# Kernel tuning notes

Measured on AMD Instinct MI355X. Metric: run time of the kernel, lower is better.

## Reference

```python
import jax, jax.numpy as jnp
import numpy as np

B, C, N, K, L = 4, 256, 8192, 4, 3


def _mlp2(h, W1, b1, W2, b2):
    return jax.nn.relu(h @ W1 + b1) @ W2 + b2


def setup_inputs() -> dict:
    key = jax.random.key(0)
    ks = jax.random.split(key, 12)
    s = lambda fan_in: 1.0 / np.sqrt(fan_in)
    inp = {
        "x": jax.random.normal(ks[0], (B, C, N), jnp.float32),
        "points": jax.random.normal(ks[1], (N, 3), jnp.float32),
        "neighbors": jax.random.randint(ks[2], (N, K), 0, N, jnp.int32),
        "edge_W1": jax.random.normal(ks[3], (3, C // 4), jnp.float32) * s(3),
        "edge_b1": jnp.zeros((C // 4,), jnp.float32),
        "edge_W2": jax.random.normal(ks[4], (C // 4, C // 2), jnp.float32) * s(C // 4),
        "edge_b2": jnp.zeros((C // 2,), jnp.float32),
        "msg_W1": jax.random.normal(ks[5], (L, 2 * C + C // 2, 2 * C), jnp.float32) * s(2 * C + C // 2),
        "msg_b1": jnp.zeros((L, 2 * C), jnp.float32),
        "msg_W2": jax.random.normal(ks[6], (L, 2 * C, C), jnp.float32) * s(2 * C),
        "msg_b2": jnp.zeros((L, C), jnp.float32),
        "upd_W1": jax.random.normal(ks[7], (L, 2 * C, 2 * C), jnp.float32) * s(2 * C),
        "upd_b1": jnp.zeros((L, 2 * C), jnp.float32),
        "upd_W2": jax.random.normal(ks[8], (L, 2 * C, C), jnp.float32) * s(2 * C),
        "upd_b2": jnp.zeros((L, C), jnp.float32),
    }
    return inp


def reference(x, points, neighbors, edge_W1, edge_b1, edge_W2, edge_b2,
              msg_W1, msg_b1, msg_W2, msg_b2, upd_W1, upd_b1, upd_W2, upd_b2):
    # x: [B, C, N] -> features [B, N, C]
    feats = jnp.transpose(x, (0, 2, 1))
    # edge features shared across layers: [N, K, C//2]
    edge_vec = points[neighbors] - points[:, None, :]          # [N, K, 3]
    edge_feat = _mlp2(edge_vec, edge_W1, edge_b1, edge_W2, edge_b2)
    for l in range(L):
        sender = feats[:, neighbors, :]                         # [B, N, K, C]
        receiver = jnp.broadcast_to(feats[:, :, None, :], sender.shape)
        ef = jnp.broadcast_to(edge_feat[None], (feats.shape[0],) + edge_feat.shape)
        msg_in = jnp.concatenate([sender, receiver, ef], axis=-1)  # [B,N,K,2.5C]
        msg = _mlp2(msg_in, msg_W1[l], msg_b1[l], msg_W2[l], msg_b2[l])
        agg = jnp.mean(msg, axis=2)                             # [B, N, C]
        upd_in = jnp.concatenate([feats, agg], axis=-1)         # [B, N, 2C]
        feats = _mlp2(upd_in, upd_W1[l], upd_b1[l], upd_W2[l], upd_b2[l])
    return jnp.transpose(feats, (0, 2, 1))
```

## Files before the change

### kernel.cpp

```cpp
#include <hip/hip_runtime.h>

#define DEVI __device__ __forceinline__

typedef unsigned short u16;
typedef unsigned int   u32;
typedef __attribute__((ext_vector_type(8))) short short8;
typedef __attribute__((ext_vector_type(4))) short short4b;
typedef __attribute__((ext_vector_type(4))) float f32x4;

DEVI float bf2f(u16 u) {
    union { u32 i; float f; } x; x.i = ((u32)u) << 16; return x.f;
}
DEVI u16 f2bf(float f) {
    u32 u = __float_as_uint(f);
    u32 r = (u + 0x7FFFu + ((u >> 16) & 1u)) >> 16;
    return (u16)r;
}

DEVI void gload_lds16(const void* g, void* l) {
    __builtin_amdgcn_global_load_lds((const __attribute__((address_space(1))) void*)g,
                                     (__attribute__((address_space(3))) void*)l, 16, 0, 0);
}

struct PJob { u32 dst, soff, tbase, ld, Kd, src; };
__device__ const PJob g_jobs[19] = {
    {0,        0,      0,    128, 64,  4},
    {8192,     0,      8,    512, 256, 0},
    {139264,   131072, 136,  512, 256, 0},
    {270336,   262144, 264,  512, 128, 0},
    {335872,   0,      328,  256, 512, 1},
    {466944,   0,      456,  512, 512, 2},
    {729088,   0,      712,  256, 512, 3},
    {860160,   327680, 840,  512, 256, 0},
    {991232,   458752, 968,  512, 256, 0},
    {1122304,  589824, 1096, 512, 128, 0},
    {1187840,  131072, 1160, 256, 512, 1},
    {1318912,  262144, 1288, 512, 512, 2},
    {1581056,  131072, 1544, 256, 512, 3},
    {1712128,  655360, 1672, 512, 256, 0},
    {1843200,  786432, 1800, 512, 256, 0},
    {1974272,  917504, 1928, 512, 128, 0},
    {2039808,  262144, 1992, 256, 512, 1},
    {2170880,  524288, 2120, 512, 512, 2},
    {2433024,  262144, 2376, 256, 512, 3},
};

__global__ void prep_weights(const float* __restrict__ mW1, const float* __restrict__ mW2,
                             const float* __restrict__ uW1, const float* __restrict__ uW2,
                             const float* __restrict__ eW2, u16* __restrict__ wreg)
{
    int bid = blockIdx.x;
    int ji = 0;
    #pragma unroll
    for (int i = 1; i < 19; ++i) if (bid >= (int)g_jobs[i].tbase) ji = i;
    PJob jb = g_jobs[ji];
    const float* src = (jb.src == 0) ? mW1 : (jb.src == 1) ? mW2 : (jb.src == 2) ? uW1
                     : (jb.src == 3) ? uW2 : eW2;
    src += jb.soff;
    int t  = bid - (int)jb.tbase;
    int nk = (int)jb.Kd >> 5;
    int tk = t % nk, tj = t / nk;
    int k0 = tk * 32, j0 = tj * 32;
    __shared__ float tile[32][33];
    int tx = threadIdx.x, ty = threadIdx.y;
    #pragma unroll
    for (int yy = 0; yy < 4; ++yy) {
        int k = k0 + ty + yy * 8;
        tile[ty + yy * 8][tx] = src[(size_t)k * jb.ld + j0 + tx];
    }
    __syncthreads();
    u16* dst = wreg + jb.dst;
    #pragma unroll
    for (int yy = 0; yy < 4; ++yy) {
        int j = j0 + ty + yy * 8;
        dst[(size_t)j * jb.Kd + k0 + tx] = f2bf(tile[tx][ty + yy * 8]);
    }
}

__global__ __launch_bounds__(256) void conv_w2(const float* __restrict__ mW2,
                                               u16* __restrict__ mW2bf)
{
    int i = blockIdx.x * 256 + threadIdx.x;
    float4 v = *(const float4*)&mW2[(size_t)i * 4];
    short4b o;
    o[0] = (short)f2bf(v.x); o[1] = (short)f2bf(v.y);
    o[2] = (short)f2bf(v.z); o[3] = (short)f2bf(v.w);
    *(short4b*)&mW2bf[(size_t)i * 4] = o;
}

__global__ __launch_bounds__(256) void biasfix(const u16* __restrict__ wreg,
    const float* __restrict__ mb2, const float* __restrict__ ub1,
    float* __restrict__ ub1c)
{
    int idx = blockIdx.x * 256 + threadIdx.x;
    int l = idx >> 9, n = idx & 511;
    const u16* U1T = wreg + 8192 + l * 851968 + 458752;
    const float* b2 = mb2 + l * 256;
    float s = ub1[l * 512 + n];
    for (int j0 = 0; j0 < 256; j0 += 8) {
        short8 wv = *(const short8*)&U1T[(size_t)n * 512 + 256 + j0];
        #pragma unroll
        for (int jj = 0; jj < 8; ++jj) s += bf2f((u16)wv[jj]) * b2[j0 + jj];
    }
    ub1c[idx] = s;
}

__global__ void transpose_in(const float* __restrict__ x, u16* __restrict__ feats)
{
    __shared__ float tile[32][33];
    int n0 = blockIdx.x * 32, c0 = blockIdx.y * 32, b = blockIdx.z;
    int tx = threadIdx.x, ty = threadIdx.y;
    #pragma unroll
    for (int yy = 0; yy < 4; ++yy) {
        int c = c0 + ty + yy * 8;
        tile[ty + yy * 8][tx] = x[((size_t)b * 256 + c) * 8192 + n0 + tx];
    }
    __syncthreads();
    #pragma unroll
    for (int yy = 0; yy < 4; ++yy) {
        int n = n0 + ty + yy * 8;
        feats[((size_t)b * 8192 + n) * 256 + c0 + tx] = f2bf(tile[tx][ty + yy * 8]);
    }
}

__global__ void transpose_out(const u16* __restrict__ feats, float* __restrict__ out)
{
    __shared__ float tile[32][33];
    int n0 = blockIdx.x * 32, c0 = blockIdx.y * 32, b = blockIdx.z;
    int tx = threadIdx.x, ty = threadIdx.y;
    #pragma unroll
    for (int yy = 0; yy < 4; ++yy) {
        int n = n0 + ty + yy * 8;
        tile[ty + yy * 8][tx] = bf2f(feats[((size_t)b * 8192 + n) * 256 + c0 + tx]);
    }
    __syncthreads();
    #pragma unroll
    for (int yy = 0; yy < 4; ++yy) {
        int c = c0 + ty + yy * 8;
        out[((size_t)b * 256 + c) * 8192 + n0 + tx] = tile[tx][ty + yy * 8];
    }
}

__global__ __launch_bounds__(256) void edge_h(
    const float* __restrict__ points, const int* __restrict__ nb,
    const float* __restrict__ W1, const float* __restrict__ b1,
    u16* __restrict__ h)
{
    int e = blockIdx.x * 256 + threadIdx.x;
    int n = e >> 2;
    int j2 = nb[e];
    float p0x = points[n * 3], p0y = points[n * 3 + 1], p0z = points[n * 3 + 2];
    float v0 = points[j2 * 3]     - p0x;
    float v1 = points[j2 * 3 + 1] - p0y;
    float v2 = points[j2 * 3 + 2] - p0z;
    #pragma unroll
    for (int jb = 0; jb < 8; ++jb) {
        short8 o;
        #pragma unroll
        for (int jj = 0; jj < 8; ++jj) {
            int j = jb * 8 + jj;
            float hv = v0 * W1[j] + v1 * W1[64 + j] + v2 * W1[128 + j] + b1[j];
            o[jj] = (short)f2bf(fmaxf(hv, 0.0f));
        }
        *(short8*)&h[(size_t)e * 64 + jb * 8] = o;
    }
}

__global__ __launch_bounds__(256) void gemm_bt(
    const u16* __restrict__ A1, int lda1, int K1,
    const u16* __restrict__ A2, int lda2,
    const u16* __restrict__ B1, int ldb1,
    const u16* __restrict__ B2, int ldb2,
    const float* __restrict__ bias,
    u16* __restrict__ Cp, int ldc,
    int nbn, int Ktot, int relu)
{
    __shared__ u16 lds[128 * 136];
    u16* At = lds;
    u16* Bt = lds + 8192;
    int nwg = (int)gridDim.x;
    int bx0 = (int)blockIdx.x;
    int bx = (bx0 & 7) * (nwg >> 3) + (bx0 >> 3);
    int tn = bx % nbn, tm = bx / nbn;
    int t = threadIdx.x;
    int l = t & 63, w = t >> 6;
    int wrow = (w >> 1) * 64, wcol = (w & 1) * 64;
    int lm = l & 15, lk = l >> 4;
    int swz = lm & 7;

    f32x4 acc[4][4];
    #pragma unroll
    for (int mi = 0; mi < 4; ++mi)
        #pragma unroll
        for (int ni = 0; ni < 4; ++ni)
            acc[mi][ni] = (f32x4){0.f, 0.f, 0.f, 0.f};

    int rowA = tm * 128;
    int rowB = tn * 128;
    int nks = Ktot >> 6;
    for (int ks = 0; ks < nks; ++ks) {
        int kg0 = ks << 6;
        bool useA1 = kg0 < K1;
        const u16* Ab = useA1 ? A1 : A2;
        const u16* Bb = useA1 ? B1 : B2;
        int lda = useA1 ? lda1 : lda2;
        int ldb = useA1 ? ldb1 : ldb2;
        int kg  = useA1 ? kg0 : kg0 - K1;
        #pragma unroll
        for (int i = 0; i < 4; ++i) {
            int chunk = i * 256 + t;
            int r = chunk >> 3, s = chunk & 7;
            int c = s ^ (r & 7);
            gload_lds16(Ab + (size_t)(rowA + r) * lda + kg + c * 8, &At[chunk * 8]);
        }
        #pragma unroll
        for (int i = 0; i < 4; ++i) {
            int chunk = i * 256 + t;
            int r = chunk >> 3, s = chunk & 7;
            int c = s ^ (r & 7);
            gload_lds16(Bb + (size_t)(rowB + r) * ldb + kg + c * 8, &Bt[chunk * 8]);
        }
        __syncthreads();
        #pragma unroll
        for (int ksub = 0; ksub < 2; ++ksub) {
            int sOff = (((ksub << 2) | lk) ^ swz) << 3;
            short8 af[4], bv[4];
            #pragma unroll
            for (int mi = 0; mi < 4; ++mi)
                af[mi] = *(const short8*)&At[(wrow + mi * 16 + lm) * 64 + sOff];
            #pragma unroll
            for (int ni = 0; ni < 4; ++ni)
                bv[ni] = *(const short8*)&Bt[(wcol + ni * 16 + lm) * 64 + sOff];
            #pragma unroll
            for (int mi = 0; mi < 4; ++mi)
                #pragma unroll
                for (int ni = 0; ni < 4; ++ni)
                    acc[mi][ni] = __builtin_amdgcn_mfma_f32_16x16x32_bf16(af[mi], bv[ni], acc[mi][ni], 0, 0, 0);
        }
        __syncthreads();
    }

    #pragma unroll
    for (int ni = 0; ni < 4; ++ni) {
        int col = wcol + ni * 16 + lm;
        float bvl = bias ? bias[tn * 128 + col] : 0.0f;
        #pragma unroll
        for (int mi = 0; mi < 4; ++mi) {
            int row0 = wrow + mi * 16 + lk * 4;
            f32x4 v = acc[mi][ni];
            #pragma unroll
            for (int r = 0; r < 4; ++r) {
                float f = v[r] + bvl;
                if (relu) f = fmaxf(f, 0.0f);
                lds[(row0 + r) * 136 + col] = f2bf(f);
            }
        }
    }
    __syncthreads();
    #pragma unroll
    for (int p = 0; p < 8; ++p) {
        int chunk = p * 256 + t;
        int row = chunk >> 4, sl = chunk & 15;
        short8 v = *(const short8*)&lds[row * 136 + sl * 8];
        *(short8*)&Cp[(size_t)(tm * 128 + row) * ldc + tn * 128 + sl * 8] = v;
    }
}

__global__ __launch_bounds__(256) void gather_relu_mean(
    const u16* __restrict__ PR, const u16* __restrict__ E,
    const int* __restrict__ nb, const float* __restrict__ b1,
    u16* __restrict__ hbar)
{
    int b = threadIdx.x >> 6, l = threadIdx.x & 63;
    int c0 = l * 8;
    int n0 = blockIdx.x * 4;

    float4 b1a = *(const float4*)&b1[c0];
    float4 b1b = *(const float4*)&b1[c0 + 4];
    float bb[8] = {b1a.x, b1a.y, b1a.z, b1a.w, b1b.x, b1b.y, b1b.z, b1b.w};

    int4 nbv[4];
    #pragma unroll
    for (int ii = 0; ii < 4; ++ii) nbv[ii] = *(const int4*)&nb[(n0 + ii) * 4];

    #pragma unroll
    for (int ii = 0; ii < 4; ++ii) {
        int n = n0 + ii;
        int m = (b << 13) + n;
        int nbarr[4] = {nbv[ii].x, nbv[ii].y, nbv[ii].z, nbv[ii].w};

        short8 rv = *(const short8*)&PR[(size_t)m * 1024 + 512 + c0];
        float base[8], acc[8];
        #pragma unroll
        for (int j = 0; j < 8; ++j) { base[j] = bf2f((u16)rv[j]) + bb[j]; acc[j] = 0.0f; }

        #pragma unroll
        for (int k = 0; k < 4; ++k) {
            short8 pv = *(const short8*)&PR[((size_t)(b << 13) + nbarr[k]) * 1024 + c0];
            short8 ev = *(const short8*)&E[(size_t)(n * 4 + k) * 512 + c0];
            #pragma unroll
            for (int j = 0; j < 8; ++j) {
                float v = bf2f((u16)pv[j]) + bf2f((u16)ev[j]) + base[j];
                acc[j] += fmaxf(v, 0.0f);
            }
        }
        short8 o;
        #pragma unroll
        for (int j = 0; j < 8; ++j) o[j] = (short)f2bf(acc[j] * 0.25f);
        *(short8*)&hbar[(size_t)m * 512 + c0] = o;
    }
}

extern "C" void kernel_launch(void* const* d_in, const int* in_sizes, int n_in,
                              void* d_out, int out_size, void* d_ws, size_t ws_size,
                              hipStream_t stream)
{
    const float* x      = (const float*)d_in[0];
    const float* points = (const float*)d_in[1];
    const int*   nb     = (const int*)d_in[2];
    const float* eW1    = (const float*)d_in[3];
    const float* eb1    = (const float*)d_in[4];
    const float* eW2    = (const float*)d_in[5];
    const float* eb2    = (const float*)d_in[6];
    const float* mW1    = (const float*)d_in[7];
    const float* mb1    = (const float*)d_in[8];
    const float* mW2    = (const float*)d_in[9];
    const float* mb2    = (const float*)d_in[10];
    const float* uW1    = (const float*)d_in[11];
    const float* ub1    = (const float*)d_in[12];
    const float* uW2    = (const float*)d_in[13];
    const float* ub2    = (const float*)d_in[14];
    float* out = (float*)d_out;

    char* ws = (char*)d_ws;
    u16* featsA = (u16*)(ws);
    u16* featsB = (u16*)(ws + 16777216);
    u16* ef     = (u16*)(ws + 33554432);
    u16* PR     = (u16*)(ws + 41943040);
    u16* E      = (u16*)(ws + 109051904);
    u16* hbar   = (u16*)(ws + 142606336);
    u16* wreg   = (u16*)(ws + 176160768);
    u16*   mW2bf = (u16*)(ws + 181288960);
    u16*   WcT   = (u16*)(ws + 182075392);
    float* ub1c  = (float*)(ws + 183648256);
    u16* hEdge  = PR;
    u16* H2     = PR;
    u16* agg    = E;

    const bool fused = (ws_size >= 183654400ull);

    prep_weights<<<2504, dim3(32, 8), 0, stream>>>(mW1, mW2, uW1, uW2, eW2, wreg);
    transpose_in<<<dim3(256, 8, 4), dim3(32, 8), 0, stream>>>(x, featsA);
    edge_h<<<128, 256, 0, stream>>>(points, nb, eW1, eb1, hEdge);
    gemm_bt<<<256, 256, 0, stream>>>(hEdge, 64, 64, hEdge, 64,
                                     wreg, 64, wreg, 64, eb2, ef, 128, 1, 64, 0);

    if (fused) {
        conv_w2<<<384, 256, 0, stream>>>(mW2, mW2bf);
        for (int l = 0; l < 3; ++l) {
            const u16* U1T = wreg + 8192 + l * 851968 + 458752;
            gemm_bt<<<16, 256, 0, stream>>>(U1T + 256, 512, 256, U1T, 512,
                                            mW2bf + l * 131072, 256, mW2bf, 256,
                                            nullptr, WcT + l * 262144, 512, 4, 256, 0);
        }
        biasfix<<<6, 256, 0, stream>>>(wreg, mb2, ub1, ub1c);
    }

    const u16* fin = featsA; u16* fout = featsB;
    for (int lyr = 0; lyr < 3; ++lyr) {
        u16* W1abT = wreg + 8192 + lyr * 851968;
        u16* W1cT  = W1abT + 262144;
        u16* W2T   = W1abT + 327680;
        u16* U1T   = W1abT + 458752;
        u16* U2T   = W1abT + 720896;
        const float* b1  = mb1 + lyr * 512;
        const float* b2  = mb2 + lyr * 256;
        const float* u1b = ub1 + lyr * 512;
        const float* u2b = ub2 + lyr * 256;

        gemm_bt<<<2048, 256, 0, stream>>>((const u16*)fin, 256, 256, (const u16*)fin, 256,
                                          W1abT, 256, W1abT, 256,
                                          nullptr, PR, 1024, 8, 256, 0);
        gemm_bt<<<1024, 256, 0, stream>>>(ef, 128, 128, ef, 128,
                                          W1cT, 128, W1cT, 128,
                                          nullptr, E, 512, 4, 128, 0);
        gather_relu_mean<<<2048, 256, 0, stream>>>(PR, E, nb, b1, hbar);

        if (fused) {
            gemm_bt<<<1024, 256, 0, stream>>>((const u16*)fin, 256, 256, hbar, 512,
                                              U1T, 512, WcT + lyr * 262144, 512,
                                              ub1c + lyr * 512, H2, 512, 4, 768, 1);
        } else {
            gemm_bt<<<512, 256, 0, stream>>>(hbar, 512, 512, hbar, 512,
                                             W2T, 512, W2T, 512,
                                             b2, agg, 256, 2, 512, 0);
            gemm_bt<<<1024, 256, 0, stream>>>((const u16*)fin, 256, 256, agg, 256,
                                              U1T, 512, U1T + 256, 512,
                                              u1b, H2, 512, 4, 512, 1);
        }
        gemm_bt<<<512, 256, 0, stream>>>(H2, 512, 512, H2, 512,
                                         U2T, 512, U2T, 512,
                                         u2b, fout, 256, 2, 512, 0);

        const u16* tmp = fin; fin = fout; fout = (u16*)tmp;
    }
    transpose_out<<<dim3(256, 8, 4), dim3(32, 8), 0, stream>>>(fin, out);
}
```

Baseline: 487.4 us.

## Double-buffer GEMM LDS tiles and interleave PR rows by batch for gather locality

The GEMM kernel now uses two LDS stages, so the next K-slice's global-to-LDS loads are issued before the MFMA work on the current slice, and MFMA sections run at raised wave priority. This hides global load latency behind compute, at the cost of double the LDS per block (64 KB), which may lower occupancy. Separately, the PR projection output is written with rows permuted to node-major, batch-minor order. The gather kernel's reads for the four batches of a node then fall in adjacent rows, which is meant to improve cache locality of the random neighbor gathers.

```diff
diff --git a/kernel.cpp b/kernel.cpp
--- a/kernel.cpp
+++ b/kernel.cpp
@@ -173,11 +173,9 @@
     const u16* __restrict__ B2, int ldb2,
     const float* __restrict__ bias,
     u16* __restrict__ Cp, int ldc,
-    int nbn, int Ktot, int relu)
-{
-    __shared__ u16 lds[128 * 136];
-    u16* At = lds;
-    u16* Bt = lds + 8192;
+    int nbn, int Ktot, int relu, int permrows)
+{
+    __shared__ u16 lds[32768];
     int nwg = (int)gridDim.x;
     int bx0 = (int)blockIdx.x;
     int bx = (bx0 & 7) * (nwg >> 3) + (bx0 >> 3);
@@ -187,6 +185,8 @@
     int wrow = (w >> 1) * 64, wcol = (w & 1) * 64;
     int lm = l & 15, lk = l >> 4;
     int swz = lm & 7;
+    int rowA = tm * 128;
+    int rowB = tn * 128;
 
     f32x4 acc[4][4];
     #pragma unroll
@@ -195,10 +195,7 @@
         for (int ni = 0; ni < 4; ++ni)
             acc[mi][ni] = (f32x4){0.f, 0.f, 0.f, 0.f};
 
-    int rowA = tm * 128;
-    int rowB = tn * 128;
-    int nks = Ktot >> 6;
-    for (int ks = 0; ks < nks; ++ks) {
+    auto STAGE = [&](int d, int ks) {
         int kg0 = ks << 6;
         bool useA1 = kg0 < K1;
         const u16* Ab = useA1 ? A1 : A2;
@@ -206,6 +203,8 @@
         int lda = useA1 ? lda1 : lda2;
         int ldb = useA1 ? ldb1 : ldb2;
         int kg  = useA1 ? kg0 : kg0 - K1;
+        u16* At = lds + d * 16384;
+        u16* Bt = At + 8192;
         #pragma unroll
         for (int i = 0; i < 4; ++i) {
             int chunk = i * 256 + t;
@@ -220,7 +219,17 @@
             int c = s ^ (r & 7);
             gload_lds16(Bb + (size_t)(rowB + r) * ldb + kg + c * 8, &Bt[chunk * 8]);
         }
-        __syncthreads();
+    };
+
+    int nks = Ktot >> 6;
+    STAGE(0, 0);
+    __syncthreads();
+    int cur = 0;
+    for (int ks = 0; ks < nks; ++ks) {
+        if (ks + 1 < nks) STAGE(cur ^ 1, ks + 1);
+        const u16* At = lds + cur * 16384;
+        const u16* Bt = At + 8192;
+        __builtin_amdgcn_s_setprio(1);
         #pragma unroll
         for (int ksub = 0; ksub < 2; ++ksub) {
             int sOff = (((ksub << 2) | lk) ^ swz) << 3;
@@ -237,7 +246,9 @@
                 for (int ni = 0; ni < 4; ++ni)
                     acc[mi][ni] = __builtin_amdgcn_mfma_f32_16x16x32_bf16(af[mi], bv[ni], acc[mi][ni], 0, 0, 0);
         }
+        __builtin_amdgcn_s_setprio(0);
         __syncthreads();
+        cur ^= 1;
     }
 
     #pragma unroll
@@ -262,7 +273,9 @@
         int chunk = p * 256 + t;
         int row = chunk >> 4, sl = chunk & 15;
         short8 v = *(const short8*)&lds[row * 136 + sl * 8];
-        *(short8*)&Cp[(size_t)(tm * 128 + row) * ldc + tn * 128 + sl * 8] = v;
+        int m = tm * 128 + row;
+        int orow = permrows ? (((m & 8191) << 2) | (m >> 13)) : m;
+        *(short8*)&Cp[(size_t)orow * ldc + tn * 128 + sl * 8] = v;
     }
 }
 
@@ -286,17 +299,16 @@
     #pragma unroll
     for (int ii = 0; ii < 4; ++ii) {
         int n = n0 + ii;
-        int m = (b << 13) + n;
         int nbarr[4] = {nbv[ii].x, nbv[ii].y, nbv[ii].z, nbv[ii].w};
 
-        short8 rv = *(const short8*)&PR[(size_t)m * 1024 + 512 + c0];
+        short8 rv = *(const short8*)&PR[(size_t)(n * 4 + b) * 1024 + 512 + c0];
         float base[8], acc[8];
         #pragma unroll
         for (int j = 0; j < 8; ++j) { base[j] = bf2f((u16)rv[j]) + bb[j]; acc[j] = 0.0f; }
 
         #pragma unroll
         for (int k = 0; k < 4; ++k) {
-            short8 pv = *(const short8*)&PR[((size_t)(b << 13) + nbarr[k]) * 1024 + c0];
+            short8 pv = *(const short8*)&PR[(size_t)(nbarr[k] * 4 + b) * 1024 + c0];
             short8 ev = *(const short8*)&E[(size_t)(n * 4 + k) * 512 + c0];
             #pragma unroll
             for (int j = 0; j < 8; ++j) {
@@ -307,7 +319,7 @@
         short8 o;
         #pragma unroll
         for (int j = 0; j < 8; ++j) o[j] = (short)f2bf(acc[j] * 0.25f);
-        *(short8*)&hbar[(size_t)m * 512 + c0] = o;
+        *(short8*)&hbar[((size_t)(b << 13) + n) * 512 + c0] = o;
     }
 }
 
@@ -353,7 +365,7 @@
     transpose_in<<<dim3(256, 8, 4), dim3(32, 8), 0, stream>>>(x, featsA);
     edge_h<<<128, 256, 0, stream>>>(points, nb, eW1, eb1, hEdge);
     gemm_bt<<<256, 256, 0, stream>>>(hEdge, 64, 64, hEdge, 64,
-                                     wreg, 64, wreg, 64, eb2, ef, 128, 1, 64, 0);
+                                     wreg, 64, wreg, 64, eb2, ef, 128, 1, 64, 0, 0);
 
     if (fused) {
         conv_w2<<<384, 256, 0, stream>>>(mW2, mW2bf);
@@ -361,7 +373,7 @@
             const u16* U1T = wreg + 8192 + l * 851968 + 458752;
             gemm_bt<<<16, 256, 0, stream>>>(U1T + 256, 512, 256, U1T, 512,
                                             mW2bf + l * 131072, 256, mW2bf, 256,
-                                            nullptr, WcT + l * 262144, 512, 4, 256, 0);
+                                            nullptr, WcT + l * 262144, 512, 4, 256, 0, 0);
         }
         biasfix<<<6, 256, 0, stream>>>(wreg, mb2, ub1, ub1c);
     }
@@ -380,27 +392,27 @@
 
         gemm_bt<<<2048, 256, 0, stream>>>((const u16*)fin, 256, 256, (const u16*)fin, 256,
                                           W1abT, 256, W1abT, 256,
-                                          nullptr, PR, 1024, 8, 256, 0);
+                                          nullptr, PR, 1024, 8, 256, 0, 1);
         gemm_bt<<<1024, 256, 0, stream>>>(ef, 128, 128, ef, 128,
                                           W1cT, 128, W1cT, 128,
-                                          nullptr, E, 512, 4, 128, 0);
+                                          nullptr, E, 512, 4, 128, 0, 0);
         gather_relu_mean<<<2048, 256, 0, stream>>>(PR, E, nb, b1, hbar);
 
         if (fused) {
             gemm_bt<<<1024, 256, 0, stream>>>((const u16*)fin, 256, 256, hbar, 512,
                                               U1T, 512, WcT + lyr * 262144, 512,
-                                              ub1c + lyr * 512, H2, 512, 4, 768, 1);
+                                              ub1c + lyr * 512, H2, 512, 4, 768, 1, 0);
         } else {
             gemm_bt<<<512, 256, 0, stream>>>(hbar, 512, 512, hbar, 512,
                                              W2T, 512, W2T, 512,
-                                             b2, agg, 256, 2, 512, 0);
+                                             b2, agg, 256, 2, 512, 0, 0);
             gemm_bt<<<1024, 256, 0, stream>>>((const u16*)fin, 256, 256, agg, 256,
                                               U1T, 512, U1T + 256, 512,
-                                              u1b, H2, 512, 4, 512, 1);
+                                              u1b, H2, 512, 4, 512, 1, 0);
         }
         gemm_bt<<<512, 256, 0, stream>>>(H2, 512, 512, H2, 512,
                                          U2T, 512, U2T, 512,
-                                         u2b, fout, 256, 2, 512, 0);
+                                         u2b, fout, 256, 2, 512, 0, 0);
 
         const u16* tmp = fin; fin = fout; fout = (u16*)tmp;
     }
```

Measured after the change: 469.8 us. -3.6%, faster.
